# Performance work log

Hardware: AMD Instinct MI355X
Metric: run time of the kernel (lower is better)

## Reference

```python
import jax, jax.numpy as jnp
import numpy as np

INPUT_DIM = 28
OUTPUT_DIM = 21
LAYER_SIZE = 64
NUM_HIDDEN = 10  # number of 64x64 hidden layers after the input layer


def setup_inputs() -> dict:
    key = jax.random.key(0)
    ks = jax.random.split(key, 7)
    x = jax.random.normal(ks[0], (1048576, INPUT_DIM), dtype=jnp.float32)
    # PyTorch nn.Linear default init: U(-1/sqrt(fan_in), 1/sqrt(fan_in)); plain uniform is fine for a baseline.
    s_in = 1.0 / np.sqrt(INPUT_DIM)
    s_h = 1.0 / np.sqrt(LAYER_SIZE)
    W_in = jax.random.uniform(ks[1], (INPUT_DIM, LAYER_SIZE), jnp.float32, -s_in, s_in)
    b_in = jax.random.uniform(ks[2], (LAYER_SIZE,), jnp.float32, -s_in, s_in)
    W_hid = jax.random.uniform(ks[3], (NUM_HIDDEN, LAYER_SIZE, LAYER_SIZE), jnp.float32, -s_h, s_h)
    b_hid = jax.random.uniform(ks[4], (NUM_HIDDEN, LAYER_SIZE), jnp.float32, -s_h, s_h)
    W_out = jax.random.uniform(ks[5], (LAYER_SIZE, OUTPUT_DIM), jnp.float32, -s_h, s_h)
    b_out = jax.random.uniform(ks[6], (OUTPUT_DIM,), jnp.float32, -s_h, s_h)
    return {"x": x, "W_in": W_in, "b_in": b_in, "W_hid": W_hid, "b_hid": b_hid,
            "W_out": W_out, "b_out": b_out}


def reference(x, W_in, b_in, W_hid, b_hid, W_out, b_out):
    h = jax.nn.relu(x @ W_in + b_in)  # [B, 64]
    def step(h, wb):
        W, b = wb
        return jax.nn.relu(h @ W + b), None
    h, _ = jax.lax.scan(step, h, (W_hid, b_hid))
    return jax.nn.sigmoid(h @ W_out + b_out)  # [B, 21]
```

## Files before the change

### kernel.cpp

```cpp
#include <hip/hip_runtime.h>

#define DEV __device__ __forceinline__
#define SBAR() __builtin_amdgcn_sched_barrier(0)

typedef _Float16 half8 __attribute__((ext_vector_type(8)));
typedef _Float16 half2v __attribute__((ext_vector_type(2)));
typedef float f32x16 __attribute__((ext_vector_type(16)));
typedef int int4v __attribute__((ext_vector_type(4)));

DEV f32x16 mfma16(half8 a, half8 b, f32x16 c) {
    return __builtin_amdgcn_mfma_f32_32x32x16_f16(a, b, c, 0, 0, 0);
}
DEV half8 h8(int4v v) { return __builtin_bit_cast(half8, v); }
DEV half8 ldh8(const _Float16* p) { return *(const half8*)p; }
DEV int pkrtz(float a, float b) {
    auto t = __builtin_amdgcn_cvt_pkrtz(a, b);
    return __builtin_bit_cast(int, t);
}
DEV int relupk(float a, float b) {
    int p = pkrtz(a, b);
    half2v h = __builtin_bit_cast(half2v, p);
    half2v z = {(_Float16)0.f, (_Float16)0.f};
    h = __builtin_elementwise_max(h, z);
    return __builtin_bit_cast(int, h);
}

DEV f32x16 zero16() {
    f32x16 z = {0.f,0.f,0.f,0.f,0.f,0.f,0.f,0.f,0.f,0.f,0.f,0.f,0.f,0.f,0.f,0.f};
    return z;
}

struct Frags { int4v c[4]; };

DEV void repack(const f32x16& C0, const f32x16& C1, Frags& B) {
    int4v b0, b1, b2, b3;
#pragma unroll
    for (int q = 0; q < 4; ++q) {
        b0[q] = relupk(C0[2*q],     C0[2*q+1]);
        b1[q] = relupk(C0[8+2*q],   C0[9+2*q]);
        b2[q] = relupk(C1[2*q],     C1[2*q+1]);
        b3[q] = relupk(C1[8+2*q],   C1[9+2*q]);
    }
    B.c[0] = b0; B.c[1] = b1; B.c[2] = b2; B.c[3] = b3;
}

DEV void loadA4(const _Float16* base, int lam, half8* A0, half8* A1) {
    const _Float16* p0 = base + lam * 8;
    const _Float16* p1 = base + 2048 + lam * 8;
#pragma unroll
    for (int kk = 0; kk < 4; ++kk) {
        A0[kk] = ldh8(p0 + kk * 512);
        A1[kk] = ldh8(p1 + kk * 512);
    }
}

DEV void biasLoad(const float* bD, int l, int h, f32x16& n0, f32x16& n1) {
    const float* p = bD + l * 64 + h * 16;
#pragma unroll
    for (int i = 0; i < 4; ++i) {
        float4 a = *(const float4*)(p + 4 * i);
        float4 b = *(const float4*)(p + 32 + 4 * i);
        n0[4*i+0] = a.x; n0[4*i+1] = a.y; n0[4*i+2] = a.z; n0[4*i+3] = a.w;
        n1[4*i+0] = b.x; n1[4*i+1] = b.y; n1[4*i+2] = b.z; n1[4*i+3] = b.w;
    }
}

DEV void mfma_hid4b(const half8* A0, const half8* A1, const Frags& Bx,
                    const f32x16& n0, const f32x16& n1, f32x16& C0, f32x16& C1) {
    __builtin_amdgcn_s_setprio(1);
    half8 b0 = h8(Bx.c[0]);
    C0 = mfma16(A0[0], b0, n0);
    C1 = mfma16(A1[0], b0, n1);
#pragma unroll
    for (int kk = 1; kk < 4; ++kk) {
        half8 b = h8(Bx.c[kk]);
        C0 = mfma16(A0[kk], b, C0);
        C1 = mfma16(A1[kk], b, C1);
    }
    __builtin_amdgcn_s_setprio(0);
}

DEV void mfma_in_t(const half8* I, const Frags& Bx, f32x16& C0, f32x16& C1) {
    __builtin_amdgcn_s_setprio(1);
    C0 = mfma16(I[0], h8(Bx.c[0]), zero16());
    C1 = mfma16(I[2], h8(Bx.c[0]), zero16());
    C0 = mfma16(I[1], h8(Bx.c[1]), C0);
    C1 = mfma16(I[3], h8(Bx.c[1]), C1);
    __builtin_amdgcn_s_setprio(0);
}

DEV void mfma_out4(const half8* Ao, const Frags& Bx, const f32x16& bo, f32x16& C) {
    __builtin_amdgcn_s_setprio(1);
    C = mfma16(Ao[0], h8(Bx.c[0]), bo);
#pragma unroll
    for (int kk = 1; kk < 4; ++kk) C = mfma16(Ao[kk], h8(Bx.c[kk]), C);
    __builtin_amdgcn_s_setprio(0);
}

DEV void store_out(const f32x16& C, int h, float* __restrict__ out, int row) {
    float* o = out + row * 21;
#pragma unroll
    for (int r = 0; r < 16; ++r) {
        int f = (r & 3) + 8 * (r >> 2) + 4 * h;
        if (f < 21) o[f] = __builtin_amdgcn_rcpf(1.f + __expf(-C[r]));
    }
}

DEV void load_x(const float* __restrict__ x, int row, int h, Frags& B) {
    const float* xr = x + row * 28;
    float4 fa = *(const float4*)(xr + 8 * h);
    float4 fb = *(const float4*)(xr + 8 * h + 4);
    float4 fc = *(const float4*)(xr + 16 + 8 * h);
    float4 fd = (h == 0) ? *(const float4*)(xr + 20) : make_float4(1.f, 0.f, 0.f, 0.f);
    int4v c0, c1;
    c0[0] = pkrtz(fa.x, fa.y); c0[1] = pkrtz(fa.z, fa.w);
    c0[2] = pkrtz(fb.x, fb.y); c0[3] = pkrtz(fb.z, fb.w);
    c1[0] = pkrtz(fc.x, fc.y); c1[1] = pkrtz(fc.z, fc.w);
    c1[2] = pkrtz(fd.x, fd.y); c1[3] = pkrtz(fd.z, fd.w);
    B.c[0] = c0; B.c[1] = c1;
}

#define NT 512

__global__ __attribute__((amdgpu_flat_work_group_size(NT, NT), amdgpu_waves_per_eu(2, 2)))
void mlp_fused(
    const float* __restrict__ x, const float* __restrict__ W_in, const float* __restrict__ b_in,
    const float* __restrict__ W_hid, const float* __restrict__ b_hid,
    const float* __restrict__ W_out, const float* __restrict__ b_out,
    float* __restrict__ out) {
    __shared__ __align__(16) _Float16 wH[40960];
    __shared__ __align__(16) _Float16 wI[2048];
    __shared__ __align__(16) _Float16 wO[2048];
    __shared__ __align__(16) float biasD[640];
    __shared__ __align__(16) float biasOut[32];

    const int tid = threadIdx.x;

    for (int i = tid; i < 2048; i += NT) { wI[i] = (_Float16)0.f; wO[i] = (_Float16)0.f; }
    __syncthreads();

    for (int i = tid; i < 40960; i += NT) {
        int o = i & 63, kin = (i >> 6) & 63, l = i >> 12;
        int m = o >> 5, kk = kin >> 4;
        int hh = (kin >> 2) & 1;
        int e = (kin & 3) + 4 * ((kin >> 3) & 1);
        int lam = hh * 32 + (o & 31);
        wH[l * 4096 + m * 2048 + kk * 512 + lam * 8 + e] = (_Float16)W_hid[i];
    }
    for (int i = tid; i < 640; i += NT) {
        int l = i >> 6, f = i & 63;
        int half = f >> 5, fin = f & 31;
        int hh = (fin >> 2) & 1, r = (fin & 3) + 4 * (fin >> 3);
        biasD[l * 64 + half * 32 + hh * 16 + r] = b_hid[i];
    }
    for (int i = tid; i < 1792; i += NT) {
        int o = i & 63, kin = i >> 6;
        int m = o >> 5, kk = kin >> 4, hh = (kin >> 3) & 1, e = kin & 7;
        int lam = hh * 32 + (o & 31);
        wI[m * 1024 + kk * 512 + lam * 8 + e] = (_Float16)W_in[i];
    }
    for (int i = tid; i < 64; i += NT) {
        int m = i >> 5;
        wI[m * 1024 + 512 + (32 + (i & 31)) * 8 + 4] = (_Float16)b_in[i];
    }
    for (int i = tid; i < 1344; i += NT) {
        int o = i % 21, kin = i / 21;
        int kk = kin >> 4;
        int hh = (kin >> 2) & 1;
        int e = (kin & 3) + 4 * ((kin >> 3) & 1);
        int lam = hh * 32 + o;
        wO[kk * 512 + lam * 8 + e] = (_Float16)W_out[i];
    }
    for (int i = tid; i < 32; i += NT) {
        int hh = i >> 4, r = i & 15;
        int f = (r & 3) + 8 * (r >> 2) + 4 * hh;
        biasOut[i] = (f < 21) ? b_out[f] : 0.f;
    }
    __syncthreads();

    const int w = tid >> 6, lam = tid & 63;
    const int col = lam & 31, h = lam >> 5;

    half8 I[4], Ao[4];
    f32x16 bo;
    {
        const _Float16* p0 = wI + lam * 8;
        const _Float16* p1 = wI + 1024 + lam * 8;
        I[0] = ldh8(p0);       I[1] = ldh8(p0 + 512);
        I[2] = ldh8(p1);       I[3] = ldh8(p1 + 512);
        const _Float16* po = wO + lam * 8;
#pragma unroll
        for (int kk = 0; kk < 4; ++kk) Ao[kk] = ldh8(po + kk * 512);
        const float* pb = biasOut + h * 16;
#pragma unroll
        for (int i = 0; i < 4; ++i) {
            float4 a = *(const float4*)(pb + 4 * i);
            bo[4*i+0] = a.x; bo[4*i+1] = a.y; bo[4*i+2] = a.z; bo[4*i+3] = a.w;
        }
    }

    const int tbase = blockIdx.x * 128;
#pragma unroll 1
    for (int j = 0; j < 8; ++j) {
        int tA = tbase + w * 16 + 2 * j;
        int rowA = tA * 32 + col, rowB = rowA + 32;
        Frags BA, BB;
        load_x(x, rowA, h, BA);
        load_x(x, rowB, h, BB);

        half8 Fa0[4], Fa1[4], Fb0[4], Fb1[4];
        f32x16 CA0, CA1, CB0, CB1;
        f32x16 nE0, nE1, nO0, nO1;

        mfma_in_t(I, BA, CA0, CA1);
        loadA4(wH, lam, Fa0, Fa1);
        biasLoad(biasD, 0, h, nE0, nE1);
        mfma_in_t(I, BB, CB0, CB1);
        repack(CA0, CA1, BA);
        SBAR();

#pragma unroll
        for (int l2 = 0; l2 < 5; ++l2) {
            const _Float16* b0 = wH + (2 * l2) * 4096;
            mfma_hid4b(Fa0, Fa1, BA, nE0, nE1, CA0, CA1);
            loadA4(b0 + 4096, lam, Fb0, Fb1);
            biasLoad(biasD, 2 * l2 + 1, h, nO0, nO1);
            repack(CB0, CB1, BB);
            SBAR();
            mfma_hid4b(Fa0, Fa1, BB, nE0, nE1, CB0, CB1);
            repack(CA0, CA1, BA);
            SBAR();
            mfma_hid4b(Fb0, Fb1, BA, nO0, nO1, CA0, CA1);
            if (l2 < 4) {
                loadA4(b0 + 8192, lam, Fa0, Fa1);
                biasLoad(biasD, 2 * l2 + 2, h, nE0, nE1);
            }
            repack(CB0, CB1, BB);
            SBAR();
            mfma_hid4b(Fb0, Fb1, BB, nO0, nO1, CB0, CB1);
            repack(CA0, CA1, BA);
            SBAR();
        }

        f32x16 CoA, CoB;
        mfma_out4(Ao, BA, bo, CoA);
        repack(CB0, CB1, BB);
        SBAR();
        mfma_out4(Ao, BB, bo, CoB);
        store_out(CoA, h, out, rowA);
        store_out(CoB, h, out, rowB);
    }
}

extern "C" void kernel_launch(void* const* d_in, const int* in_sizes, int n_in,
                              void* d_out, int out_size, void* d_ws, size_t ws_size,
                              hipStream_t stream) {
    const float* x     = (const float*)d_in[0];
    const float* W_in  = (const float*)d_in[1];
    const float* b_in  = (const float*)d_in[2];
    const float* W_hid = (const float*)d_in[3];
    const float* b_hid = (const float*)d_in[4];
    const float* W_out = (const float*)d_in[5];
    const float* b_out = (const float*)d_in[6];
    float* out = (float*)d_out;
    mlp_fused<<<dim3(256), dim3(NT), 0, stream>>>(x, W_in, b_in, W_hid, b_hid, W_out, b_out, out);
}
```

Measured before the change: 97.32 us.

## Process four row tiles per wave with 256-thread blocks and one wave per EU

Halves the block to 256 threads (one wave per SIMD) and has each wave interleave four 32-row tiles instead of two through all layers. Each weight fragment loaded from LDS now feeds four MFMA chains, which reduces LDS traffic per row and gives more independent MFMA work to hide latency within a single wave. The cost is much higher register pressure (eight f32x16 accumulators plus four B fragments) and less latency hiding from other waves, with a risk of spills.

```diff
diff --git a/kernel.cpp b/kernel.cpp
--- a/kernel.cpp
+++ b/kernel.cpp
@@ -120,9 +120,9 @@
     B.c[0] = c0; B.c[1] = c1;
 }
 
-#define NT 512
-
-__global__ __attribute__((amdgpu_flat_work_group_size(NT, NT), amdgpu_waves_per_eu(2, 2)))
+#define NT 256
+
+__global__ __attribute__((amdgpu_flat_work_group_size(NT, NT), amdgpu_waves_per_eu(1, 1)))
 void mlp_fused(
     const float* __restrict__ x, const float* __restrict__ W_in, const float* __restrict__ b_in,
     const float* __restrict__ W_hid, const float* __restrict__ b_hid,
@@ -202,14 +202,17 @@
     const int tbase = blockIdx.x * 128;
 #pragma unroll 1
     for (int j = 0; j < 8; ++j) {
-        int tA = tbase + w * 16 + 2 * j;
-        int rowA = tA * 32 + col, rowB = rowA + 32;
-        Frags BA, BB;
+        int t0 = tbase + w * 32 + 4 * j;
+        int rowA = (t0 + 0) * 32 + col, rowB = (t0 + 1) * 32 + col;
+        int rowC = (t0 + 2) * 32 + col, rowD = (t0 + 3) * 32 + col;
+        Frags BA, BB, BC, BD;
         load_x(x, rowA, h, BA);
         load_x(x, rowB, h, BB);
+        load_x(x, rowC, h, BC);
+        load_x(x, rowD, h, BD);
 
         half8 Fa0[4], Fa1[4], Fb0[4], Fb1[4];
-        f32x16 CA0, CA1, CB0, CB1;
+        f32x16 CA0, CA1, CB0, CB1, CC0, CC1, CD0, CD1;
         f32x16 nE0, nE1, nO0, nO1;
 
         mfma_in_t(I, BA, CA0, CA1);
@@ -218,6 +221,12 @@
         mfma_in_t(I, BB, CB0, CB1);
         repack(CA0, CA1, BA);
         SBAR();
+        mfma_in_t(I, BC, CC0, CC1);
+        repack(CB0, CB1, BB);
+        SBAR();
+        mfma_in_t(I, BD, CD0, CD1);
+        repack(CC0, CC1, BC);
+        SBAR();
 
 #pragma unroll
         for (int l2 = 0; l2 < 5; ++l2) {
@@ -225,30 +234,48 @@
             mfma_hid4b(Fa0, Fa1, BA, nE0, nE1, CA0, CA1);
             loadA4(b0 + 4096, lam, Fb0, Fb1);
             biasLoad(biasD, 2 * l2 + 1, h, nO0, nO1);
-            repack(CB0, CB1, BB);
+            repack(CD0, CD1, BD);
             SBAR();
             mfma_hid4b(Fa0, Fa1, BB, nE0, nE1, CB0, CB1);
             repack(CA0, CA1, BA);
+            SBAR();
+            mfma_hid4b(Fa0, Fa1, BC, nE0, nE1, CC0, CC1);
+            repack(CB0, CB1, BB);
+            SBAR();
+            mfma_hid4b(Fa0, Fa1, BD, nE0, nE1, CD0, CD1);
+            repack(CC0, CC1, BC);
             SBAR();
             mfma_hid4b(Fb0, Fb1, BA, nO0, nO1, CA0, CA1);
             if (l2 < 4) {
                 loadA4(b0 + 8192, lam, Fa0, Fa1);
                 biasLoad(biasD, 2 * l2 + 2, h, nE0, nE1);
             }
-            repack(CB0, CB1, BB);
+            repack(CD0, CD1, BD);
             SBAR();
             mfma_hid4b(Fb0, Fb1, BB, nO0, nO1, CB0, CB1);
             repack(CA0, CA1, BA);
             SBAR();
+            mfma_hid4b(Fb0, Fb1, BC, nO0, nO1, CC0, CC1);
+            repack(CB0, CB1, BB);
+            SBAR();
+            mfma_hid4b(Fb0, Fb1, BD, nO0, nO1, CD0, CD1);
+            repack(CC0, CC1, BC);
+            SBAR();
         }
 
-        f32x16 CoA, CoB;
+        f32x16 CoA, CoB, CoC, CoD;
         mfma_out4(Ao, BA, bo, CoA);
-        repack(CB0, CB1, BB);
+        repack(CD0, CD1, BD);
         SBAR();
         mfma_out4(Ao, BB, bo, CoB);
         store_out(CoA, h, out, rowA);
+        SBAR();
+        mfma_out4(Ao, BC, bo, CoC);
         store_out(CoB, h, out, rowB);
+        SBAR();
+        mfma_out4(Ao, BD, bo, CoD);
+        store_out(CoC, h, out, rowC);
+        store_out(CoD, h, out, rowD);
     }
 }
 
```

Result: slower. 134.2 us (+37.9%).
